# Kernel tuning notes

Hardware: AMD Instinct MI355X
Metric: run time of the kernel (lower is better)

Reference implementation:

```python
import jax, jax.numpy as jnp
import numpy as np

B, S, E, FF = 8, 16384, 256, 1024
H, W, G = 128, 128, 16
Hn, Wn = H // G, W // G


def setup_inputs() -> dict:
    key = jax.random.key(0)
    ks = jax.random.split(key, 16)
    w = lambda k, shape: jax.random.normal(k, shape, jnp.float32) * 0.02
    return {
        "x": jax.random.normal(ks[0], (B, S, E), jnp.float32),
        "Wq": w(ks[1], (E, E)), "bq": jnp.zeros((E,), jnp.float32),
        "Wk": w(ks[2], (E, E)), "bk": jnp.zeros((E,), jnp.float32),
        "Wv": w(ks[3], (E, E)), "bv": jnp.zeros((E,), jnp.float32),
        "Wo": w(ks[4], (E, E)), "bo": jnp.zeros((E,), jnp.float32),
        "W1": w(ks[5], (E, FF)), "b1": jnp.zeros((FF,), jnp.float32),
        "W2": w(ks[6], (FF, E)), "b2": jnp.zeros((E,), jnp.float32),
        "g1": jnp.ones((E,), jnp.float32), "be1": jnp.zeros((E,), jnp.float32),
        "g2": jnp.ones((E,), jnp.float32), "be2": jnp.zeros((E,), jnp.float32),
    }


def _ln(x, g, b, eps=1e-5):
    m = jnp.mean(x, axis=-1, keepdims=True)
    v = jnp.mean(jnp.square(x - m), axis=-1, keepdims=True)
    return (x - m) * jax.lax.rsqrt(v + eps) * g + b


def _forward(x, Wq, bq, Wk, bk, Wv, bv, Wo, bo, W1, b1, W2, b2, g1, be1, g2, be2):
    # x: (B, S, E) -> (B, E, H, W), faithful to torch reshape (row-major reinterpret)
    x4 = x.reshape(B, E, H, W)
    # window partition: each window is the contiguous (E, G, G) block the torch loop slices
    xw = x4.reshape(B, E, Hn, G, Wn, G).transpose(0, 2, 4, 1, 3, 5)  # (B,Hn,Wn,E,G,G)
    # faithful raw reinterpretation (E,G,G) -> (G*G, E), matching grid.reshape(B,-1,E)
    t = xw.reshape(B, Hn * Wn, G * G, E)  # (B, nW, T=256, E)
    # single-head self-attention per window (batched over all windows at once)
    q = jnp.einsum('bwte,ef->bwtf', t, Wq) + bq
    k = jnp.einsum('bwte,ef->bwtf', t, Wk) + bk
    v = jnp.einsum('bwte,ef->bwtf', t, Wv) + bv
    scores = jnp.einsum('bwqe,bwke->bwqk', q, k) / jnp.sqrt(jnp.float32(E))
    attn = jax.nn.softmax(scores, axis=-1)
    o = jnp.einsum('bwqk,bwke->bwqe', attn, v)
    o = jnp.einsum('bwte,ef->bwtf', o, Wo) + bo  # (B, nW, 256, E)
    # reverse: view each window back to (E,G,G) and reassemble the feature map
    y = o.reshape(B, Hn, Wn, E, G, G).transpose(0, 3, 1, 4, 2, 5).reshape(B, E, H, W)
    y = y.reshape(B, S, E)  # faithful x.view(B, -1, E)
    # FFN (dropout is identity in eval) + residual with post-LN as written
    h = jax.nn.gelu(jnp.einsum('bse,ef->bsf', y, W1) + b1, approximate=False)
    ffn = jnp.einsum('bsf,fe->bse', h, W2) + b2
    y = y + _ln(ffn, g1, be1)
    y = y + _ln(y, g2, be2)
    return y


def reference(x, Wq, bq, Wk, bk, Wv, bv, Wo, bo, W1, b1, W2, b2, g1, be1, g2, be2):
    return _forward(x, Wq, bq, Wk, bk, Wv, bv, Wo, bo, W1, b1, W2, b2, g1, be1, g2, be2)
```

## Files before the change

### kernel.cpp

```cpp
#include <hip/hip_runtime.h>
#include <hip/hip_bf16.h>


typedef __bf16 bf16x8 __attribute__((ext_vector_type(8)));
typedef float  f32x4  __attribute__((ext_vector_type(4)));
typedef unsigned short us16;
typedef us16 us16x8 __attribute__((ext_vector_type(8)));
typedef us16 us16x4 __attribute__((ext_vector_type(4)));
typedef us16 us16x2 __attribute__((ext_vector_type(2)));

#define DI static __device__ __forceinline__

DI us16 f2b(float f){ __bf16 h = (__bf16)f; return __builtin_bit_cast(us16, h); }

DI bf16x8 cvt8(f32x4 a, f32x4 b){
  bf16x8 r;
  r[0]=(__bf16)a[0]; r[1]=(__bf16)a[1]; r[2]=(__bf16)a[2]; r[3]=(__bf16)a[3];
  r[4]=(__bf16)b[0]; r[5]=(__bf16)b[1]; r[6]=(__bf16)b[2]; r[7]=(__bf16)b[3];
  return r;
}
DI bf16x8 ld8(const us16* p){
  us16x8 v = *(const us16x8*)p;
  return __builtin_bit_cast(bf16x8, v);
}
DI f32x4 mfma16(bf16x8 a, bf16x8 b, f32x4 c){
  return __builtin_amdgcn_mfma_f32_16x16x32_bf16(a, b, c, 0, 0, 0);
}

DI bf16x8 ld_sw8(const char* base, int row, int f0){
  return ld8((const us16*)(base + row*512 + ((((f0>>3) ^ (row&7))) << 4)));
}
DI void st_sw1(char* base, int row, int f, us16 v){
  *(us16*)(base + row*512 + ((((f>>3) ^ (row&7))) << 4) + (f&7)*2) = v;
}
DI void st_sw4(char* base, int row, int f0, us16x4 v){
  *(us16x4*)(base + row*512 + ((((f0>>3) ^ (row&7))) << 4) + (f0&7)*2) = v;
}

DI bf16x8 ld_vt(const char* base, int row, int gg){
  return ld8((const us16*)(base + row*64 + (((gg ^ ((row>>1)&3))) << 4)));
}
DI void st_vt(char* base, int row, int col, us16 v){
  int c = col >> 3;
  *(us16*)(base + row*64 + (((c ^ ((row>>1)&3))) << 4) + (col&7)*2) = v;
}

__global__ void prep_w(const float* __restrict__ src, us16* __restrict__ dst,
                       int R, int C, int cshift){
  int idx = blockIdx.x*256 + threadIdx.x;
  if(idx >= R*C) return;
  int r = idx >> cshift;
  int c = idx & (C-1);
  dst[(size_t)c*R + r] = f2b(src[idx]);
}

__global__ __launch_bounds__(256, 2)
void qkv_win(const float* __restrict__ x,
             const us16* __restrict__ WqT, const us16* __restrict__ WkT,
             const us16* __restrict__ WvT,
             const float* __restrict__ bq, const float* __restrict__ bk,
             const float* __restrict__ bv,
             char* __restrict__ Qimg,
             char* __restrict__ KV)
{
  __shared__ __align__(16) char smem[65536];
  const int tid = threadIdx.x;
  const int wl = tid >> 6, lane = tid & 63, l15 = lane & 15, g = lane >> 4;
  const int blk = blockIdx.x;
  const int hw = blk & 1, tg = (blk>>1)&7, wh = (blk>>4)&7, b = blk>>7;
  const int win = wh*8 + hw*4 + wl;

  {
    const float* xb = x + (size_t)b*4194304 + (size_t)(tg*32)*16384 + wh*2048 + hw*64;
    const int prow = tid >> 4, pc = tid & 15;
    char* abase = smem + (pc>>2)*16384;
    const int f0 = prow*16 + (pc&3)*4;
    for(int t=0; t<32; t++){
      f32x4 v = *(const f32x4*)(xb + (size_t)t*16384 + prow*128 + pc*4);
      us16x4 pk; pk[0]=f2b(v[0]); pk[1]=f2b(v[1]); pk[2]=f2b(v[2]); pk[3]=f2b(v[3]);
      st_sw4(abase, t, f0, pk);
    }
  }
  __syncthreads();
  bf16x8 tA[2][8];
  #pragma unroll
  for(int mi=0; mi<2; mi++)
    #pragma unroll
    for(int kk=0; kk<8; kk++)
      tA[mi][kk] = ld_sw8(smem + wl*16384, mi*16 + l15, kk*32 + g*8);
  __syncthreads();

  char* outb = smem + wl*16384;
  const size_t wslot = (size_t)(b*64 + win);

  for(int n0=0; n0<16; n0++){
    f32x4 a0 = {0,0,0,0}, a1 = {0,0,0,0};
    const us16* wrow = WqT + (size_t)(n0*16 + l15)*256;
    #pragma unroll
    for(int kk=0; kk<8; kk++){
      bf16x8 wb = ld8(wrow + kk*32 + g*8);
      a0 = mfma16(tA[0][kk], wb, a0);
      a1 = mfma16(tA[1][kk], wb, a1);
    }
    float bias = bq[n0*16 + l15];
    #pragma unroll
    for(int r=0; r<4; r++){
      st_sw1(outb, g*4+r,    n0*16+l15, f2b(a0[r] + bias));
      st_sw1(outb, 16+g*4+r, n0*16+l15, f2b(a1[r] + bias));
    }
  }
  asm volatile("" ::: "memory");
  {
    char* dst = Qimg + (wslot*8 + tg)*16384;
    #pragma unroll
    for(int i=0; i<16; i++)
      *(us16x8*)(dst + i*1024 + lane*16) = *(const us16x8*)(outb + i*1024 + lane*16);
  }
  asm volatile("" ::: "memory");

  for(int n0=0; n0<16; n0++){
    f32x4 a0 = {0,0,0,0}, a1 = {0,0,0,0};
    const us16* wrow = WkT + (size_t)(n0*16 + l15)*256;
    #pragma unroll
    for(int kk=0; kk<8; kk++){
      bf16x8 wb = ld8(wrow + kk*32 + g*8);
      a0 = mfma16(tA[0][kk], wb, a0);
      a1 = mfma16(tA[1][kk], wb, a1);
    }
    float bias = bk[n0*16 + l15];
    #pragma unroll
    for(int r=0; r<4; r++){
      st_sw1(outb, g*4+r,    n0*16+l15, f2b(a0[r] + bias));
      st_sw1(outb, 16+g*4+r, n0*16+l15, f2b(a1[r] + bias));
    }
  }
  asm volatile("" ::: "memory");
  {
    char* dst = KV + wslot*262144 + tg*16384;
    #pragma unroll
    for(int i=0; i<16; i++)
      *(us16x8*)(dst + i*1024 + lane*16) = *(const us16x8*)(outb + i*1024 + lane*16);
  }
  asm volatile("" ::: "memory");

  for(int n0=0; n0<16; n0++){
    f32x4 a0 = {0,0,0,0}, a1 = {0,0,0,0};
    const us16* wrow = WvT + (size_t)(n0*16 + l15)*256;
    f32x4 bv4 = *(const f32x4*)(bv + n0*16 + g*4);
    #pragma unroll
    for(int kk=0; kk<8; kk++){
      bf16x8 wa = ld8(wrow + kk*32 + g*8);
      a0 = mfma16(wa, tA[0][kk], a0);
      a1 = mfma16(wa, tA[1][kk], a1);
    }
    #pragma unroll
    for(int r=0; r<4; r++){
      int jr = n0*16 + g*4 + r;
      st_vt(outb, jr, l15,      f2b(a0[r] + bv4[r]));
      st_vt(outb, jr, 16 + l15, f2b(a1[r] + bv4[r]));
    }
  }
  asm volatile("" ::: "memory");
  {
    char* dst = KV + wslot*262144 + 131072 + tg*16384;
    #pragma unroll
    for(int i=0; i<16; i++)
      *(us16x8*)(dst + i*1024 + lane*16) = *(const us16x8*)(outb + i*1024 + lane*16);
  }
}

__global__ __launch_bounds__(256, 2)
void kv_win(const float* __restrict__ x,
            const us16* __restrict__ WkT, const us16* __restrict__ WvT,
            const float* __restrict__ bk, const float* __restrict__ bv,
            char* __restrict__ KV)
{
  __shared__ __align__(16) char smem[65536];
  const int tid = threadIdx.x;
  const int wl = tid >> 6, lane = tid & 63, l15 = lane & 15, g = lane >> 4;
  const int blk = blockIdx.x;
  const int hw = blk & 1, tg = (blk>>1)&7, wh = (blk>>4)&7, b = blk>>7;
  const int win = wh*8 + hw*4 + wl;

  {
    const float* xb = x + (size_t)b*4194304 + (size_t)(tg*32)*16384 + wh*2048 + hw*64;
    const int prow = tid >> 4, pc = tid & 15;
    char* abase = smem + (pc>>2)*16384;
    const int f0 = prow*16 + (pc&3)*4;
    for(int t=0; t<32; t++){
      f32x4 v = *(const f32x4*)(xb + (size_t)t*16384 + prow*128 + pc*4);
      us16x4 pk; pk[0]=f2b(v[0]); pk[1]=f2b(v[1]); pk[2]=f2b(v[2]); pk[3]=f2b(v[3]);
      st_sw4(abase, t, f0, pk);
    }
  }
  __syncthreads();
  bf16x8 tA[2][8];
  #pragma unroll
  for(int mi=0; mi<2; mi++)
    #pragma unroll
    for(int kk=0; kk<8; kk++)
      tA[mi][kk] = ld_sw8(smem + wl*16384, mi*16 + l15, kk*32 + g*8);
  __syncthreads();

  char* outb = smem + wl*16384;
  const size_t wslot = (size_t)(b*64 + win);

  for(int n0=0; n0<16; n0++){
    f32x4 a0 = {0,0,0,0}, a1 = {0,0,0,0};
    const us16* wrow = WkT + (size_t)(n0*16 + l15)*256;
    #pragma unroll
    for(int kk=0; kk<8; kk++){
      bf16x8 wb = ld8(wrow + kk*32 + g*8);
      a0 = mfma16(tA[0][kk], wb, a0);
      a1 = mfma16(tA[1][kk], wb, a1);
    }
    float bias = bk[n0*16 + l15];
    #pragma unroll
    for(int r=0; r<4; r++){
      st_sw1(outb, g*4+r,    n0*16+l15, f2b(a0[r] + bias));
      st_sw1(outb, 16+g*4+r, n0*16+l15, f2b(a1[r] + bias));
    }
  }
  asm volatile("" ::: "memory");
  {
    char* dst = KV + wslot*262144 + tg*16384;
    #pragma unroll
    for(int i=0; i<16; i++)
      *(us16x8*)(dst + i*1024 + lane*16) = *(const us16x8*)(outb + i*1024 + lane*16);
  }
  asm volatile("" ::: "memory");

  for(int n0=0; n0<16; n0++){
    f32x4 a0 = {0,0,0,0}, a1 = {0,0,0,0};
    const us16* wrow = WvT + (size_t)(n0*16 + l15)*256;
    f32x4 bv4 = *(const f32x4*)(bv + n0*16 + g*4);
    #pragma unroll
    for(int kk=0; kk<8; kk++){
      bf16x8 wa = ld8(wrow + kk*32 + g*8);
      a0 = mfma16(wa, tA[0][kk], a0);
      a1 = mfma16(wa, tA[1][kk], a1);
    }
    #pragma unroll
    for(int r=0; r<4; r++){
      int jr = n0*16 + g*4 + r;
      st_vt(outb, jr, l15,      f2b(a0[r] + bv4[r]));
      st_vt(outb, jr, 16 + l15, f2b(a1[r] + bv4[r]));
    }
  }
  asm volatile("" ::: "memory");
  {
    char* dst = KV + wslot*262144 + 131072 + tg*16384;
    #pragma unroll
    for(int i=0; i<16; i++)
      *(us16x8*)(dst + i*1024 + lane*16) = *(const us16x8*)(outb + i*1024 + lane*16);
  }
}

DI void load_kv_regs(const char* slot, int kt, us16x8* r, int wid, int lane){
  const char* src = (wid < 4)
      ? slot + (size_t)kt*16384 + wid*4096
      : slot + 131072 + (size_t)kt*16384 + (wid-4)*4096;
  #pragma unroll
  for(int i=0; i<4; i++)
    r[i] = *(const us16x8*)(src + i*1024 + lane*16);
}
DI void write_kv_lds(char* kb, char* vb, const us16x8* r, int wid, int lane){
  char* dst = (wid < 4) ? kb + wid*4096 : vb + (wid-4)*4096;
  #pragma unroll
  for(int i=0; i<4; i++)
    *(us16x8*)(dst + i*1024 + lane*16) = r[i];
}

DI void attn_core_loop(char* smem, us16* Psw, const char* slot,
                       const bf16x8 Qf[2][8], us16x8* stg,
                       const us16* WoT, const float* bo, float* yb,
                       int wid, int lane, int l15, int g, int r0)
{
  us16* Qw = (us16*)(smem) + wid*(32*264);
  float mr0 = -1e30f, mr1 = -1e30f, lr0 = 0.f, lr1 = 0.f;
  f32x4 Ot[16][2];
  const f32x4 zf = {0,0,0,0};
  #pragma unroll
  for(int i=0;i<16;i++){ Ot[i][0]=zf; Ot[i][1]=zf; }
  __syncthreads();

  for(int kt=0; kt<8; kt++){
    char* kb = (kt&1) ? smem + 16384 : smem;
    char* vb = (kt&1) ? smem + 49152 : smem + 32768;
    if(kt < 7) load_kv_regs(slot, kt+1, stg, wid, lane);
    f32x4 st[2][2] = {{zf,zf},{zf,zf}};
    #pragma unroll
    for(int kk=0; kk<8; kk++){
      int f0 = kk*32 + g*8;
      bf16x8 k0 = ld_sw8(kb, l15, f0);
      bf16x8 k1 = ld_sw8(kb, 16 + l15, f0);
      st[0][0] = mfma16(k0, Qf[0][kk], st[0][0]);
      st[0][1] = mfma16(k0, Qf[1][kk], st[0][1]);
      st[1][0] = mfma16(k1, Qf[0][kk], st[1][0]);
      st[1][1] = mfma16(k1, Qf[1][kk], st[1][1]);
    }
    #pragma unroll
    for(int mi=0; mi<2; mi++)
      #pragma unroll
      for(int qn=0; qn<2; qn++)
        #pragma unroll
        for(int r=0; r<4; r++) st[mi][qn][r] *= 0.0625f;
    float tm0 = st[0][0][0], tm1 = st[0][1][0];
    #pragma unroll
    for(int mi=0; mi<2; mi++)
      #pragma unroll
      for(int r=0; r<4; r++){
        tm0 = fmaxf(tm0, st[mi][0][r]);
        tm1 = fmaxf(tm1, st[mi][1][r]);
      }
    tm0 = fmaxf(tm0, __shfl_xor(tm0, 16)); tm0 = fmaxf(tm0, __shfl_xor(tm0, 32));
    tm1 = fmaxf(tm1, __shfl_xor(tm1, 16)); tm1 = fmaxf(tm1, __shfl_xor(tm1, 32));
    float mn0 = fmaxf(mr0, tm0), mn1 = fmaxf(mr1, tm1);
    float c0 = __expf(mr0 - mn0), c1 = __expf(mr1 - mn1);
    float ts0 = 0.f, ts1 = 0.f;
    #pragma unroll
    for(int mi=0; mi<2; mi++)
      #pragma unroll
      for(int r=0; r<4; r++){
        float p0 = __expf(st[mi][0][r] - mn0); st[mi][0][r] = p0; ts0 += p0;
        float p1 = __expf(st[mi][1][r] - mn1); st[mi][1][r] = p1; ts1 += p1;
      }
    ts0 += __shfl_xor(ts0, 16); ts0 += __shfl_xor(ts0, 32);
    ts1 += __shfl_xor(ts1, 16); ts1 += __shfl_xor(ts1, 32);
    lr0 = lr0*c0 + ts0;  lr1 = lr1*c1 + ts1;  mr0 = mn0;  mr1 = mn1;
    #pragma unroll
    for(int i=0;i<16;i++){
      #pragma unroll
      for(int r=0;r<4;r++){ Ot[i][0][r] *= c0; Ot[i][1][r] *= c1; }
    }
    #pragma unroll
    for(int qn=0; qn<2; qn++)
      #pragma unroll
      for(int mi=0; mi<2; mi++)
        #pragma unroll
        for(int rp=0; rp<2; rp++){
          us16x2 pk;
          pk[0] = f2b(st[mi][qn][rp*2]);
          pk[1] = f2b(st[mi][qn][rp*2+1]);
          *(us16x2*)((char*)Psw + (qn*16 + l15)*80 + (mi*16 + g*4 + rp*2)*2) = pk;
        }
    asm volatile("" ::: "memory");
    bf16x8 pb0 = ld8(Psw + l15*40 + g*8);
    bf16x8 pb1 = ld8(Psw + (16 + l15)*40 + g*8);
    #pragma unroll
    for(int fm=0; fm<16; fm++){
      bf16x8 va = ld_vt(vb, fm*16 + l15, g);
      Ot[fm][0] = mfma16(va, pb0, Ot[fm][0]);
      Ot[fm][1] = mfma16(va, pb1, Ot[fm][1]);
    }
    if(kt < 7){
      char* kbn = (kt&1) ? smem : smem + 16384;
      char* vbn = (kt&1) ? smem + 32768 : smem + 49152;
      write_kv_lds(kbn, vbn, stg, wid, lane);
    }
    __syncthreads();
  }

  float inv0 = 1.f/lr0, inv1 = 1.f/lr1;
  #pragma unroll
  for(int fm=0; fm<16; fm++)
    #pragma unroll
    for(int rp=0; rp<2; rp++){
      us16x2 p0, p1;
      p0[0]=f2b(Ot[fm][0][rp*2]*inv0);   p0[1]=f2b(Ot[fm][0][rp*2+1]*inv0);
      p1[0]=f2b(Ot[fm][1][rp*2]*inv1);   p1[1]=f2b(Ot[fm][1][rp*2+1]*inv1);
      *(us16x2*)((char*)Qw + l15*528      + (fm*16 + g*4 + rp*2)*2) = p0;
      *(us16x2*)((char*)Qw + (16+l15)*528 + (fm*16 + g*4 + rp*2)*2) = p1;
    }
  asm volatile("" ::: "memory");
  bf16x8 Of[2][8];
  #pragma unroll
  for(int qm=0; qm<2; qm++)
    #pragma unroll
    for(int kk=0; kk<8; kk++)
      Of[qm][kk] = ld8(Qw + (qm*16 + l15)*264 + kk*32 + g*8);
  for(int n0=0; n0<16; n0++){
    f32x4 a0 = {0,0,0,0}, a1 = {0,0,0,0};
    const us16* wrow = WoT + (size_t)(n0*16 + l15)*256;
    #pragma unroll
    for(int kk=0; kk<8; kk++){
      bf16x8 wb = ld8(wrow + kk*32 + g*8);
      a0 = mfma16(Of[0][kk], wb, a0);
      a1 = mfma16(Of[1][kk], wb, a1);
    }
    float bias = bo[n0*16 + l15];
    #pragma unroll
    for(int r=0; r<4; r++){
      yb[(size_t)(r0 + g*4 + r)*16384      + n0*128 + l15] = a0[r] + bias;
      yb[(size_t)(r0 + 16 + g*4 + r)*16384 + n0*128 + l15] = a1[r] + bias;
    }
  }
}

__global__ __launch_bounds__(512, 2)
void attn_hyb2(const char* __restrict__ Qimg, const char* __restrict__ KV,
               const us16* __restrict__ WoT, const float* __restrict__ bo,
               float* __restrict__ y)
{
  __shared__ __align__(16) char smem[135168];
  const int tid = threadIdx.x, wid = tid>>6, lane = tid&63, l15 = lane&15, g = lane>>4;
  const int blk = blockIdx.x;
  const int b   = blk >> 6;
  const int win = blk & 63;
  const size_t base = (size_t)b*4194304 + (size_t)(win>>3)*2048 + (size_t)(win&7)*16;
  float*       yb = y + base;
  const char*  slot = KV + (size_t)blk*262144;
  const char*  Qt = Qimg + ((size_t)blk*8 + wid)*16384;
  us16* Psw = (us16*)(smem + 65536) + wid*1280;
  const int r0 = wid*32;

  us16x8 stg[4];
  load_kv_regs(slot, 0, stg, wid, lane);

  bf16x8 Qf[2][8];
  #pragma unroll
  for(int qn=0; qn<2; qn++)
    #pragma unroll
    for(int kk=0; kk<8; kk++){
      int row = qn*16 + l15;
      Qf[qn][kk] = ld8((const us16*)(Qt + row*512 + ((((kk*4+g) ^ (l15&7))) << 4)));
    }

  write_kv_lds(smem, smem + 32768, stg, wid, lane);
  attn_core_loop(smem, Psw, slot, Qf, stg, WoT, bo, yb, wid, lane, l15, g, r0);
}

__global__ __launch_bounds__(512, 2)
void attn_hyb(const float* __restrict__ x,
              const us16* __restrict__ WqT, const float* __restrict__ bq,
              const char* __restrict__ KV,
              const us16* __restrict__ WoT, const float* __restrict__ bo,
              float* __restrict__ y)
{
  __shared__ __align__(16) char smem[135168];
  const int tid = threadIdx.x, wid = tid>>6, lane = tid&63, l15 = lane&15, g = lane>>4;
  const int blk = blockIdx.x;
  const int b   = blk >> 6;
  const int win = blk & 63;
  const size_t base = (size_t)b*4194304 + (size_t)(win>>3)*2048 + (size_t)(win&7)*16;
  const float* xb = x + base;
  float*       yb = y + base;
  const char*  slot = KV + (size_t)blk*262144;

  us16* Qw  = (us16*)(smem) + wid*(32*264);
  us16* Psw = (us16*)(smem + 65536) + wid*1280;
  const int r0 = wid*32;

  us16x8 stg[4];
  load_kv_regs(slot, 0, stg, wid, lane);

  bf16x8 tA[2][8];
  #pragma unroll
  for(int mi=0; mi<2; mi++){
    const float* trow = xb + (size_t)(r0 + mi*16 + l15)*16384;
    #pragma unroll
    for(int kk=0; kk<8; kk++){
      int f0 = kk*32 + g*8;
      const float* p = trow + (f0>>4)*128 + (f0&15);
      tA[mi][kk] = cvt8(*(const f32x4*)p, *(const f32x4*)(p+4));
    }
  }
  for(int n0=0; n0<16; n0++){
    f32x4 a0 = {0,0,0,0}, a1 = {0,0,0,0};
    const us16* wrow = WqT + (size_t)(n0*16 + l15)*256;
    #pragma unroll
    for(int kk=0; kk<8; kk++){
      bf16x8 wb = ld8(wrow + kk*32 + g*8);
      a0 = mfma16(tA[0][kk], wb, a0);
      a1 = mfma16(tA[1][kk], wb, a1);
    }
    float bias = bq[n0*16 + l15];
    #pragma unroll
    for(int r=0; r<4; r++){
      Qw[(g*4+r)*264      + n0*16 + l15] = f2b(a0[r] + bias);
      Qw[(16+g*4+r)*264   + n0*16 + l15] = f2b(a1[r] + bias);
    }
  }
  asm volatile("" ::: "memory");
  bf16x8 Qf[2][8];
  #pragma unroll
  for(int qn=0; qn<2; qn++)
    #pragma unroll
    for(int kk=0; kk<8; kk++)
      Qf[qn][kk] = ld8(Qw + (qn*16 + l15)*264 + kk*32 + g*8);
  __syncthreads();

  write_kv_lds(smem, smem + 32768, stg, wid, lane);
  attn_core_loop(smem, Psw, slot, Qf, stg, WoT, bo, yb, wid, lane, l15, g, r0);
}

__global__ __launch_bounds__(512, 2)
void ffn_ln(float* y,
            const us16* __restrict__ W1T, const us16* __restrict__ W2T,
            const float* __restrict__ b1, const float* __restrict__ b2,
            const float* __restrict__ g1, const float* __restrict__ be1,
            const float* __restrict__ g2, const float* __restrict__ be2)
{
  __shared__ __align__(16) char smem[132096];
  us16*  h  = (us16*)smem;
  float* fl = (float*)smem;
  const int tid = threadIdx.x, wid = tid>>6, lane = tid&63, l15 = lane&15, g = lane>>4;
  float* Y = y + (size_t)blockIdx.x*64*256;

  bf16x8 ya[4][8];
  #pragma unroll
  for(int mi=0; mi<4; mi++){
    const float* p = Y + (size_t)(mi*16 + l15)*256;
    #pragma unroll
    for(int kk=0; kk<8; kk++){
      int f0 = kk*32 + g*8;
      ya[mi][kk] = cvt8(*(const f32x4*)(p + f0), *(const f32x4*)(p + f0 + 4));
    }
  }
  const f32x4 zf = {0,0,0,0};
  #pragma unroll 2
  for(int n0=0; n0<8; n0++){
    int j = wid*128 + n0*16 + l15;
    f32x4 acc[4] = {zf,zf,zf,zf};
    const us16* wrow = W1T + (size_t)j*256;
    #pragma unroll
    for(int kk=0; kk<8; kk++){
      bf16x8 wb = ld8(wrow + kk*32 + g*8);
      #pragma unroll
      for(int mi=0; mi<4; mi++) acc[mi] = mfma16(ya[mi][kk], wb, acc[mi]);
    }
    float bias = b1[j];
    #pragma unroll
    for(int mi=0; mi<4; mi++)
      #pragma unroll
      for(int r=0; r<4; r++){
        float v = acc[mi][r] + bias;
        v = 0.5f*v*(1.f + erff(v*0.70710678118654752f));
        h[(mi*16 + g*4 + r)*1032 + j] = f2b(v);
      }
  }
  __syncthreads();
  f32x4 acc2[4][2] = {{zf,zf},{zf,zf},{zf,zf},{zf,zf}};
  #pragma unroll 2
  for(int kk=0; kk<32; kk++){
    int f0 = kk*32 + g*8;
    bf16x8 ha[4];
    #pragma unroll
    for(int mi=0; mi<4; mi++) ha[mi] = ld8(h + (mi*16 + l15)*1032 + f0);
    #pragma unroll
    for(int n=0; n<2; n++){
      bf16x8 wb = ld8(W2T + (size_t)(wid*32 + n*16 + l15)*1024 + f0);
      #pragma unroll
      for(int mi=0; mi<4; mi++) acc2[mi][n] = mfma16(ha[mi], wb, acc2[mi][n]);
    }
  }
  __syncthreads();
  #pragma unroll
  for(int mi=0; mi<4; mi++)
    #pragma unroll
    for(int n=0; n<2; n++){
      float bias = b2[wid*32 + n*16 + l15];
      #pragma unroll
      for(int r=0; r<4; r++)
        fl[(mi*16 + g*4 + r)*260 + wid*32 + n*16 + l15] = acc2[mi][n][r] + bias;
    }
  __syncthreads();
  f32x4 G1  = *(const f32x4*)(g1  + lane*4);
  f32x4 BE1 = *(const f32x4*)(be1 + lane*4);
  f32x4 G2  = *(const f32x4*)(g2  + lane*4);
  f32x4 BE2 = *(const f32x4*)(be2 + lane*4);
  for(int rr=0; rr<8; rr++){
    int row = wid*8 + rr;
    f32x4 f  = *(const f32x4*)(fl + row*260 + lane*4);
    f32x4 yv = *(const f32x4*)(Y + (size_t)row*256 + lane*4);
    float s  = f[0]+f[1]+f[2]+f[3];
    float s2 = f[0]*f[0]+f[1]*f[1]+f[2]*f[2]+f[3]*f[3];
    #pragma unroll
    for(int m=1; m<=32; m<<=1){ s += __shfl_xor(s, m); s2 += __shfl_xor(s2, m); }
    float mu = s*(1.f/256.f);
    float rs = rsqrtf(fmaxf(s2*(1.f/256.f) - mu*mu, 0.f) + 1e-5f);
    f32x4 y1;
    #pragma unroll
    for(int i=0; i<4; i++) y1[i] = yv[i] + (f[i]-mu)*rs*G1[i] + BE1[i];
    float t1 = y1[0]+y1[1]+y1[2]+y1[3];
    float t2 = y1[0]*y1[0]+y1[1]*y1[1]+y1[2]*y1[2]+y1[3]*y1[3];
    #pragma unroll
    for(int m=1; m<=32; m<<=1){ t1 += __shfl_xor(t1, m); t2 += __shfl_xor(t2, m); }
    float mu2 = t1*(1.f/256.f);
    float rs2 = rsqrtf(fmaxf(t2*(1.f/256.f) - mu2*mu2, 0.f) + 1e-5f);
    f32x4 o;
    #pragma unroll
    for(int i=0; i<4; i++) o[i] = y1[i] + (y1[i]-mu2)*rs2*G2[i] + BE2[i];
    *(f32x4*)(Y + (size_t)row*256 + lane*4) = o;
  }
}

__global__ __launch_bounds__(512, 2)
void attn_win(const float* __restrict__ x,
              const us16* __restrict__ WqT, const us16* __restrict__ WkT,
              const us16* __restrict__ WvT, const us16* __restrict__ WoT,
              const float* __restrict__ bq, const float* __restrict__ bk,
              const float* __restrict__ bv, const float* __restrict__ bo,
              float* __restrict__ y)
{
  __shared__ __align__(16) char smem[135168];
  const int tid = threadIdx.x;
  const int wid = tid >> 6;
  const int lane = tid & 63;
  const int l15 = lane & 15;
  const int g = lane >> 4;

  const int blk = blockIdx.x;
  const int b   = blk >> 6;
  const int win = blk & 63;
  const size_t base = (size_t)b*4194304 + (size_t)(win>>3)*2048 + (size_t)(win&7)*16;
  const float* xb = x + base;
  float*       yb = y + base;

  us16* Qw    = (us16*)(smem) + wid*(32*264);
  char* slabb = smem;
  char* kldsb = smem + 16384;
  us16* Vt    = (us16*)(smem + 32768);
  us16* Psw   = (us16*)(smem + 53248) + wid*1280;

  const int r0 = wid*32;

  bf16x8 tA[2][8];
  #pragma unroll
  for(int mi=0; mi<2; mi++){
    const float* trow = xb + (size_t)(r0 + mi*16 + l15)*16384;
    #pragma unroll
    for(int kk=0; kk<8; kk++){
      int f0 = kk*32 + g*8;
      const float* p = trow + (f0>>4)*128 + (f0&15);
      tA[mi][kk] = cvt8(*(const f32x4*)p, *(const f32x4*)(p+4));
    }
  }
  for(int n0=0; n0<16; n0++){
    f32x4 a0 = {0,0,0,0}, a1 = {0,0,0,0};
    const us16* wrow = WqT + (size_t)(n0*16 + l15)*256;
    #pragma unroll
    for(int kk=0; kk<8; kk++){
      bf16x8 wb = ld8(wrow + kk*32 + g*8);
      a0 = mfma16(tA[0][kk], wb, a0);
      a1 = mfma16(tA[1][kk], wb, a1);
    }
    float bias = bq[n0*16 + l15];
    #pragma unroll
    for(int r=0; r<4; r++){
      Qw[(g*4+r)*264      + n0*16 + l15] = f2b(a0[r] + bias);
      Qw[(16+g*4+r)*264   + n0*16 + l15] = f2b(a1[r] + bias);
    }
  }
  asm volatile("" ::: "memory");
  bf16x8 Qf[2][8];
  #pragma unroll
  for(int qn=0; qn<2; qn++)
    #pragma unroll
    for(int kk=0; kk<8; kk++)
      Qf[qn][kk] = ld8(Qw + (qn*16 + l15)*264 + kk*32 + g*8);
  __syncthreads();

  const float bkv0 = bk[wid*32 + l15], bkv1 = bk[wid*32 + 16 + l15];
  float bvv[2][4];
  #pragma unroll
  for(int m=0; m<2; m++)
    #pragma unroll
    for(int r=0; r<4; r++)
      bvv[m][r] = bv[wid*32 + m*16 + g*4 + r];

  float mr0 = -1e30f, mr1 = -1e30f, lr0 = 0.f, lr1 = 0.f;
  f32x4 Ot[16][2];
  const f32x4 zf = {0,0,0,0};
  #pragma unroll
  for(int i=0;i<16;i++){ Ot[i][0]=zf; Ot[i][1]=zf; }

  for(int kt=0; kt<8; kt++){
    const int kr0 = kt*32;
    {
      int row = tid >> 4, c = tid & 15;
      const float* trow = xb + (size_t)(kr0 + row)*16384;
      #pragma unroll
      for(int j=0; j<4; j++){
        int f0 = (c + 16*j)*4;
        const float* p = trow + (f0>>4)*128 + (f0&15);
        f32x4 v = *(const f32x4*)p;
        us16x4 pk; pk[0]=f2b(v[0]); pk[1]=f2b(v[1]); pk[2]=f2b(v[2]); pk[3]=f2b(v[3]);
        st_sw4(slabb, row, f0, pk);
      }
    }
    __syncthreads();
    {
      f32x4 acc[2][2] = {{zf,zf},{zf,zf}};
      #pragma unroll
      for(int kk=0; kk<8; kk++){
        int f0 = kk*32 + g*8;
        bf16x8 a0 = ld_sw8(slabb, l15, f0);
        bf16x8 a1 = ld_sw8(slabb, 16 + l15, f0);
        #pragma unroll
        for(int n=0; n<2; n++){
          bf16x8 wb = ld8(WkT + (size_t)(wid*32 + n*16 + l15)*256 + f0);
          acc[n][0] = mfma16(a0, wb, acc[n][0]);
          acc[n][1] = mfma16(a1, wb, acc[n][1]);
        }
      }
      #pragma unroll
      for(int n=0; n<2; n++){
        float bias = n ? bkv1 : bkv0;
        #pragma unroll
        for(int r=0; r<4; r++){
          st_sw1(kldsb, g*4+r,      wid*32 + n*16 + l15, f2b(acc[n][0][r] + bias));
          st_sw1(kldsb, 16+g*4+r,   wid*32 + n*16 + l15, f2b(acc[n][1][r] + bias));
        }
      }
    }
    {
      f32x4 acc[2][2] = {{zf,zf},{zf,zf}};
      #pragma unroll
      for(int kk=0; kk<8; kk++){
        int f0 = kk*32 + g*8;
        bf16x8 b0 = ld_sw8(slabb, l15, f0);
        bf16x8 b1 = ld_sw8(slabb, 16 + l15, f0);
        #pragma unroll
        for(int fm=0; fm<2; fm++){
          bf16x8 wa = ld8(WvT + (size_t)(wid*32 + fm*16 + l15)*256 + f0);
          acc[fm][0] = mfma16(wa, b0, acc[fm][0]);
          acc[fm][1] = mfma16(wa, b1, acc[fm][1]);
        }
      }
      #pragma unroll
      for(int fm=0; fm<2; fm++)
        #pragma unroll
        for(int n=0; n<2; n++)
          #pragma unroll
          for(int r=0; r<4; r++){
            int f = wid*32 + fm*16 + g*4 + r;
            Vt[f*40 + n*16 + l15] = f2b(acc[fm][n][r] + bvv[fm][r]);
          }
    }
    __syncthreads();
    f32x4 st[2][2] = {{zf,zf},{zf,zf}};
    #pragma unroll
    for(int kk=0; kk<8; kk++){
      int f0 = kk*32 + g*8;
      bf16x8 k0 = ld_sw8(kldsb, l15, f0);
      bf16x8 k1 = ld_sw8(kldsb, 16 + l15, f0);
      st[0][0] = mfma16(k0, Qf[0][kk], st[0][0]);
      st[0][1] = mfma16(k0, Qf[1][kk], st[0][1]);
      st[1][0] = mfma16(k1, Qf[0][kk], st[1][0]);
      st[1][1] = mfma16(k1, Qf[1][kk], st[1][1]);
    }
    #pragma unroll
    for(int mi=0; mi<2; mi++)
      #pragma unroll
      for(int qn=0; qn<2; qn++)
        #pragma unroll
        for(int r=0; r<4; r++) st[mi][qn][r] *= 0.0625f;
    float tm0 = st[0][0][0], tm1 = st[0][1][0];
    #pragma unroll
    for(int mi=0; mi<2; mi++)
      #pragma unroll
      for(int r=0; r<4; r++){
        tm0 = fmaxf(tm0, st[mi][0][r]);
        tm1 = fmaxf(tm1, st[mi][1][r]);
      }
    tm0 = fmaxf(tm0, __shfl_xor(tm0, 16)); tm0 = fmaxf(tm0, __shfl_xor(tm0, 32));
    tm1 = fmaxf(tm1, __shfl_xor(tm1, 16)); tm1 = fmaxf(tm1, __shfl_xor(tm1, 32));
    float mn0 = fmaxf(mr0, tm0), mn1 = fmaxf(mr1, tm1);
    float c0 = __expf(mr0 - mn0), c1 = __expf(mr1 - mn1);
    float ts0 = 0.f, ts1 = 0.f;
    #pragma unroll
    for(int mi=0; mi<2; mi++)
      #pragma unroll
      for(int r=0; r<4; r++){
        float p0 = __expf(st[mi][0][r] - mn0); st[mi][0][r] = p0; ts0 += p0;
        float p1 = __expf(st[mi][1][r] - mn1); st[mi][1][r] = p1; ts1 += p1;
      }
    ts0 += __shfl_xor(ts0, 16); ts0 += __shfl_xor(ts0, 32);
    ts1 += __shfl_xor(ts1, 16); ts1 += __shfl_xor(ts1, 32);
    lr0 = lr0*c0 + ts0;  lr1 = lr1*c1 + ts1;  mr0 = mn0;  mr1 = mn1;
    #pragma unroll
    for(int i=0;i<16;i++){
      #pragma unroll
      for(int r=0;r<4;r++){ Ot[i][0][r] *= c0; Ot[i][1][r] *= c1; }
    }
    #pragma unroll
    for(int qn=0; qn<2; qn++)
      #pragma unroll
      for(int mi=0; mi<2; mi++)
        #pragma unroll
        for(int rp=0; rp<2; rp++){
          us16x2 pk;
          pk[0] = f2b(st[mi][qn][rp*2]);
          pk[1] = f2b(st[mi][qn][rp*2+1]);
          *(us16x2*)((char*)Psw + (qn*16 + l15)*80 + (mi*16 + g*4 + rp*2)*2) = pk;
        }
    asm volatile("" ::: "memory");
    bf16x8 pb0 = ld8(Psw + l15*40 + g*8);
    bf16x8 pb1 = ld8(Psw + (16 + l15)*40 + g*8);
    #pragma unroll
    for(int fm=0; fm<16; fm++){
      bf16x8 va = ld8(Vt + (fm*16 + l15)*40 + g*8);
      Ot[fm][0] = mfma16(va, pb0, Ot[fm][0]);
      Ot[fm][1] = mfma16(va, pb1, Ot[fm][1]);
    }
    __syncthreads();
  }

  float inv0 = 1.f/lr0, inv1 = 1.f/lr1;
  #pragma unroll
  for(int fm=0; fm<16; fm++)
    #pragma unroll
    for(int rp=0; rp<2; rp++){
      us16x2 p0, p1;
      p0[0]=f2b(Ot[fm][0][rp*2]*inv0);   p0[1]=f2b(Ot[fm][0][rp*2+1]*inv0);
      p1[0]=f2b(Ot[fm][1][rp*2]*inv1);   p1[1]=f2b(Ot[fm][1][rp*2+1]*inv1);
      *(us16x2*)((char*)Qw + l15*528      + (fm*16 + g*4 + rp*2)*2) = p0;
      *(us16x2*)((char*)Qw + (16+l15)*528 + (fm*16 + g*4 + rp*2)*2) = p1;
    }
  asm volatile("" ::: "memory");
  bf16x8 Of[2][8];
  #pragma unroll
  for(int qm=0; qm<2; qm++)
    #pragma unroll
    for(int kk=0; kk<8; kk++)
      Of[qm][kk] = ld8(Qw + (qm*16 + l15)*264 + kk*32 + g*8);
  for(int n0=0; n0<16; n0++){
    f32x4 a0 = {0,0,0,0}, a1 = {0,0,0,0};
    const us16* wrow = WoT + (size_t)(n0*16 + l15)*256;
    #pragma unroll
    for(int kk=0; kk<8; kk++){
      bf16x8 wb = ld8(wrow + kk*32 + g*8);
      a0 = mfma16(Of[0][kk], wb, a0);
      a1 = mfma16(Of[1][kk], wb, a1);
    }
    float bias = bo[n0*16 + l15];
    #pragma unroll
    for(int r=0; r<4; r++){
      yb[(size_t)(r0 + g*4 + r)*16384      + n0*128 + l15] = a0[r] + bias;
      yb[(size_t)(r0 + 16 + g*4 + r)*16384 + n0*128 + l15] = a1[r] + bias;
    }
  }
}

extern "C" void kernel_launch(void* const* d_in, const int* in_sizes, int n_in,
                              void* d_out, int out_size, void* d_ws, size_t ws_size,
                              hipStream_t stream)
{
  const float* x   = (const float*)d_in[0];
  const float* Wq  = (const float*)d_in[1];
  const float* bq  = (const float*)d_in[2];
  const float* Wk  = (const float*)d_in[3];
  const float* bk  = (const float*)d_in[4];
  const float* Wv  = (const float*)d_in[5];
  const float* bv  = (const float*)d_in[6];
  const float* Wo  = (const float*)d_in[7];
  const float* bo  = (const float*)d_in[8];
  const float* W1  = (const float*)d_in[9];
  const float* b1  = (const float*)d_in[10];
  const float* W2  = (const float*)d_in[11];
  const float* b2  = (const float*)d_in[12];
  const float* g1  = (const float*)d_in[13];
  const float* be1 = (const float*)d_in[14];
  const float* g2  = (const float*)d_in[15];
  const float* be2 = (const float*)d_in[16];
  float* out = (float*)d_out;
  char* ws = (char*)d_ws;

  const size_t KVBYTES = 134217728ull;
  const size_t QBYTES  = 67108864ull;
  const size_t NEED_B  = KVBYTES + 1572864ull;
  const size_t NEED_A  = KVBYTES + QBYTES + 1572864ull;

  if(ws_size >= NEED_A){
    char* Qimg  = ws + KVBYTES;
    char* wbase = ws + KVBYTES + QBYTES;
    us16* WqT = (us16*)(wbase);
    us16* WkT = (us16*)(wbase + 131072);
    us16* WvT = (us16*)(wbase + 262144);
    us16* WoT = (us16*)(wbase + 393216);
    us16* W1T = (us16*)(wbase + 524288);
    us16* W2T = (us16*)(wbase + 1048576);

    prep_w<<<dim3(256),  dim3(256), 0, stream>>>(Wq, WqT, 256, 256, 8);
    prep_w<<<dim3(256),  dim3(256), 0, stream>>>(Wk, WkT, 256, 256, 8);
    prep_w<<<dim3(256),  dim3(256), 0, stream>>>(Wv, WvT, 256, 256, 8);
    prep_w<<<dim3(256),  dim3(256), 0, stream>>>(Wo, WoT, 256, 256, 8);
    prep_w<<<dim3(1024), dim3(256), 0, stream>>>(W1, W1T, 256, 1024, 10);
    prep_w<<<dim3(1024), dim3(256), 0, stream>>>(W2, W2T, 1024, 256, 8);

    qkv_win<<<dim3(1024), dim3(256), 0, stream>>>(x, WqT, WkT, WvT, bq, bk, bv,
                                                  Qimg, ws);
    attn_hyb2<<<dim3(512), dim3(512), 0, stream>>>(Qimg, ws, WoT, bo, out);
    ffn_ln<<<dim3(2048), dim3(512), 0, stream>>>(out, W1T, W2T, b1, b2,
                                                 g1, be1, g2, be2);
  } else if(ws_size >= NEED_B){
    char* wbase = ws + KVBYTES;
    us16* WqT = (us16*)(wbase);
    us16* WkT = (us16*)(wbase + 131072);
    us16* WvT = (us16*)(wbase + 262144);
    us16* WoT = (us16*)(wbase + 393216);
    us16* W1T = (us16*)(wbase + 524288);
    us16* W2T = (us16*)(wbase + 1048576);

    prep_w<<<dim3(256),  dim3(256), 0, stream>>>(Wq, WqT, 256, 256, 8);
    prep_w<<<dim3(256),  dim3(256), 0, stream>>>(Wk, WkT, 256, 256, 8);
    prep_w<<<dim3(256),  dim3(256), 0, stream>>>(Wv, WvT, 256, 256, 8);
    prep_w<<<dim3(256),  dim3(256), 0, stream>>>(Wo, WoT, 256, 256, 8);
    prep_w<<<dim3(1024), dim3(256), 0, stream>>>(W1, W1T, 256, 1024, 10);
    prep_w<<<dim3(1024), dim3(256), 0, stream>>>(W2, W2T, 1024, 256, 8);

    kv_win<<<dim3(1024), dim3(256), 0, stream>>>(x, WkT, WvT, bk, bv, ws);
    attn_hyb<<<dim3(512), dim3(512), 0, stream>>>(x, WqT, bq, ws, WoT, bo, out);
    ffn_ln<<<dim3(2048), dim3(512), 0, stream>>>(out, W1T, W2T, b1, b2,
                                                 g1, be1, g2, be2);
  } else {
    us16* WqT = (us16*)(ws);
    us16* WkT = (us16*)(ws + 131072);
    us16* WvT = (us16*)(ws + 262144);
    us16* WoT = (us16*)(ws + 393216);
    us16* W1T = (us16*)(ws + 524288);
    us16* W2T = (us16*)(ws + 1048576);

    prep_w<<<dim3(256),  dim3(256), 0, stream>>>(Wq, WqT, 256, 256, 8);
    prep_w<<<dim3(256),  dim3(256), 0, stream>>>(Wk, WkT, 256, 256, 8);
    prep_w<<<dim3(256),  dim3(256), 0, stream>>>(Wv, WvT, 256, 256, 8);
    prep_w<<<dim3(256),  dim3(256), 0, stream>>>(Wo, WoT, 256, 256, 8);
    prep_w<<<dim3(1024), dim3(256), 0, stream>>>(W1, W1T, 256, 1024, 10);
    prep_w<<<dim3(1024), dim3(256), 0, stream>>>(W2, W2T, 1024, 256, 8);

    attn_win<<<dim3(512), dim3(512), 0, stream>>>(x, WqT, WkT, WvT, WoT,
                                                  bq, bk, bv, bo, out);
    ffn_ln<<<dim3(2048), dim3(512), 0, stream>>>(out, W1T, W2T, b1, b2,
                                                 g1, be1, g2, be2);
  }
}
```

Measured before the change: 825.4 us.

## Split FFN+LayerNorm into 64-row and 32-row tile kernels

```diff
diff --git a/kernel.cpp b/kernel.cpp
--- a/kernel.cpp
+++ b/kernel.cpp
@@ -43,6 +43,13 @@
 DI void st_vt(char* base, int row, int col, us16 v){
   int c = col >> 3;
   *(us16*)(base + row*64 + (((c ^ ((row>>1)&3))) << 4) + (col&7)*2) = v;
+}
+
+DI void st_h1s(char* base, int row, int f, us16 v){
+  *(us16*)(base + row*2048 + ((((f>>3) ^ (row&7))) << 4) + (f&7)*2) = v;
+}
+DI bf16x8 ld_h8s(const char* base, int row, int f0){
+  return ld8((const us16*)(base + row*2048 + ((((f0>>3) ^ (row&7))) << 4)));
 }
 
 __global__ void prep_w(const float* __restrict__ src, us16* __restrict__ dst,
@@ -60,8 +67,7 @@
              const us16* __restrict__ WvT,
              const float* __restrict__ bq, const float* __restrict__ bk,
              const float* __restrict__ bv,
-             char* __restrict__ Qimg,
-             char* __restrict__ KV)
+             char* __restrict__ Qimg, char* __restrict__ KV)
 {
   __shared__ __align__(16) char smem[65536];
   const int tid = threadIdx.x;
@@ -571,6 +577,104 @@
   f32x4 BE2 = *(const f32x4*)(be2 + lane*4);
   for(int rr=0; rr<8; rr++){
     int row = wid*8 + rr;
+    f32x4 f  = *(const f32x4*)(fl + row*260 + lane*4);
+    f32x4 yv = *(const f32x4*)(Y + (size_t)row*256 + lane*4);
+    float s  = f[0]+f[1]+f[2]+f[3];
+    float s2 = f[0]*f[0]+f[1]*f[1]+f[2]*f[2]+f[3]*f[3];
+    #pragma unroll
+    for(int m=1; m<=32; m<<=1){ s += __shfl_xor(s, m); s2 += __shfl_xor(s2, m); }
+    float mu = s*(1.f/256.f);
+    float rs = rsqrtf(fmaxf(s2*(1.f/256.f) - mu*mu, 0.f) + 1e-5f);
+    f32x4 y1;
+    #pragma unroll
+    for(int i=0; i<4; i++) y1[i] = yv[i] + (f[i]-mu)*rs*G1[i] + BE1[i];
+    float t1 = y1[0]+y1[1]+y1[2]+y1[3];
+    float t2 = y1[0]*y1[0]+y1[1]*y1[1]+y1[2]*y1[2]+y1[3]*y1[3];
+    #pragma unroll
+    for(int m=1; m<=32; m<<=1){ t1 += __shfl_xor(t1, m); t2 += __shfl_xor(t2, m); }
+    float mu2 = t1*(1.f/256.f);
+    float rs2 = rsqrtf(fmaxf(t2*(1.f/256.f) - mu2*mu2, 0.f) + 1e-5f);
+    f32x4 o;
+    #pragma unroll
+    for(int i=0; i<4; i++) o[i] = y1[i] + (y1[i]-mu2)*rs2*G2[i] + BE2[i];
+    *(f32x4*)(Y + (size_t)row*256 + lane*4) = o;
+  }
+}
+
+__global__ __launch_bounds__(512, 2)
+void ffn_ln32s(float* y,
+               const us16* __restrict__ W1T, const us16* __restrict__ W2T,
+               const float* __restrict__ b1, const float* __restrict__ b2,
+               const float* __restrict__ g1, const float* __restrict__ be1,
+               const float* __restrict__ g2, const float* __restrict__ be2)
+{
+  __shared__ __align__(16) char smem[65536];
+  float* fl = (float*)smem;
+  const int tid = threadIdx.x, wid = tid>>6, lane = tid&63, l15 = lane&15, g = lane>>4;
+  float* Y = y + (size_t)blockIdx.x*32*256;
+
+  bf16x8 ya[2][8];
+  #pragma unroll
+  for(int mi=0; mi<2; mi++){
+    const float* p = Y + (size_t)(mi*16 + l15)*256;
+    #pragma unroll
+    for(int kk=0; kk<8; kk++){
+      int f0 = kk*32 + g*8;
+      ya[mi][kk] = cvt8(*(const f32x4*)(p + f0), *(const f32x4*)(p + f0 + 4));
+    }
+  }
+  const f32x4 zf = {0,0,0,0};
+  for(int n0=0; n0<8; n0++){
+    int j = wid*128 + n0*16 + l15;
+    f32x4 acc[2] = {zf,zf};
+    const us16* wrow = W1T + (size_t)j*256;
+    #pragma unroll
+    for(int kk=0; kk<8; kk++){
+      bf16x8 wb = ld8(wrow + kk*32 + g*8);
+      #pragma unroll
+      for(int mi=0; mi<2; mi++) acc[mi] = mfma16(ya[mi][kk], wb, acc[mi]);
+    }
+    float bias = b1[j];
+    #pragma unroll
+    for(int mi=0; mi<2; mi++)
+      #pragma unroll
+      for(int r=0; r<4; r++){
+        float v = acc[mi][r] + bias;
+        v = 0.5f*v*(1.f + erff(v*0.70710678118654752f));
+        st_h1s(smem, mi*16 + g*4 + r, j, f2b(v));
+      }
+  }
+  __syncthreads();
+  f32x4 acc2[2][2] = {{zf,zf},{zf,zf}};
+  for(int kk=0; kk<32; kk++){
+    int f0 = kk*32 + g*8;
+    bf16x8 ha[2];
+    #pragma unroll
+    for(int mi=0; mi<2; mi++) ha[mi] = ld_h8s(smem, mi*16 + l15, f0);
+    #pragma unroll
+    for(int n=0; n<2; n++){
+      bf16x8 wb = ld8(W2T + (size_t)(wid*32 + n*16 + l15)*1024 + f0);
+      #pragma unroll
+      for(int mi=0; mi<2; mi++) acc2[mi][n] = mfma16(ha[mi], wb, acc2[mi][n]);
+    }
+  }
+  __syncthreads();
+  #pragma unroll
+  for(int mi=0; mi<2; mi++)
+    #pragma unroll
+    for(int n=0; n<2; n++){
+      float bias = b2[wid*32 + n*16 + l15];
+      #pragma unroll
+      for(int r=0; r<4; r++)
+        fl[(mi*16 + g*4 + r)*260 + wid*32 + n*16 + l15] = acc2[mi][n][r] + bias;
+    }
+  __syncthreads();
+  f32x4 G1  = *(const f32x4*)(g1  + lane*4);
+  f32x4 BE1 = *(const f32x4*)(be1 + lane*4);
+  f32x4 G2  = *(const f32x4*)(g2  + lane*4);
+  f32x4 BE2 = *(const f32x4*)(be2 + lane*4);
+  for(int rr=0; rr<4; rr++){
+    int row = wid*4 + rr;
     f32x4 f  = *(const f32x4*)(fl + row*260 + lane*4);
     f32x4 yv = *(const f32x4*)(Y + (size_t)row*256 + lane*4);
     float s  = f[0]+f[1]+f[2]+f[3];
@@ -892,8 +996,11 @@
     qkv_win<<<dim3(1024), dim3(256), 0, stream>>>(x, WqT, WkT, WvT, bq, bk, bv,
                                                   Qimg, ws);
     attn_hyb2<<<dim3(512), dim3(512), 0, stream>>>(Qimg, ws, WoT, bo, out);
-    ffn_ln<<<dim3(2048), dim3(512), 0, stream>>>(out, W1T, W2T, b1, b2,
+    ffn_ln<<<dim3(1024), dim3(512), 0, stream>>>(out, W1T, W2T, b1, b2,
                                                  g1, be1, g2, be2);
+    ffn_ln32s<<<dim3(2048), dim3(512), 0, stream>>>(out + 16777216ull,
+                                                    W1T, W2T, b1, b2,
+                                                    g1, be1, g2, be2);
   } else if(ws_size >= NEED_B){
     char* wbase = ws + KVBYTES;
     us16* WqT = (us16*)(wbase);
```

After: 925.3 us. 1.12x slower.
